# Kernel tuning notes

Hardware: AMD Instinct MI355X
Metric: run time of the kernel (lower is better)

The kernel has to match this reference:

```python
import jax, jax.numpy as jnp
import numpy as np

DEPTH = 4  # signature truncation depth
B, L, D = 64, 2048, 8  # batch, path length, channels


def _exp_levels(z, depth):
    """Restricted tensor exponential of a single linear increment.

    z: (B, d). Returns tuple of flattened z^{(x)k} / k!, shapes (B, d**k).
    """
    b = z.shape[0]
    levels = [z]
    for k in range(2, depth + 1):
        prev = levels[-1]  # (B, d**(k-1))
        levels.append((prev[:, :, None] * z[:, None, :]).reshape(b, -1) / k)
    return tuple(levels)


def _signature(path, depth):
    """Truncated path signature of a piecewise-linear path.

    Signature = product (in the truncated tensor algebra) of exp(increment_i),
    combined left-to-right via Chen's identity.
    path: (B, L, d) -> (B, d + d^2 + ... + d^depth)
    """
    inc = path[:, 1:, :] - path[:, :-1, :]  # (B, L-1, d)
    b = path.shape[0]

    def chen_mul_exp(A, z):
        # (A tensor-product exp(z)) truncated at `depth`.
        # C_k = A_k + e_k + sum_{j=1}^{k-1} A_{k-j} (x) e_j,  e_j = z^{(x)j}/j!
        e = _exp_levels(z, depth)
        out = []
        for k in range(1, depth + 1):
            c = A[k - 1] + e[k - 1]
            for j in range(1, k):
                c = c + (A[k - j - 1][:, :, None] * e[j - 1][:, None, :]).reshape(b, -1)
            out.append(c)
        return tuple(out)

    init = _exp_levels(inc[:, 0], depth)          # signature of first segment
    rest = jnp.swapaxes(inc[:, 1:], 0, 1)          # (L-2, B, d), scan over time
    final, _ = jax.lax.scan(lambda c, z: (chen_mul_exp(c, z), None), init, rest)
    return jnp.concatenate(final, axis=-1)         # flatten: (B, d + ... + d^depth)


def setup_inputs() -> dict:
    key = jax.random.key(0)
    path = jax.random.normal(key, (B, L, D), dtype=jnp.float32)
    return {"path": path}


def reference(path):
    return _signature(path, DEPTH)
```

## Files before the change

kernel.cpp:

```cpp
#include <hip/hip_runtime.h>

#define D8      8
#define LPATH   2048
#define NBATCH  64
#define NSTEPS  2047
#define NCHUNK  32
#define CSTEPS  64
#define SIGLEN  4680
#define OFF2    8
#define OFF3    72
#define OFF4    584
#define P4      68
#define SIGP    (OFF4 + 64 * P4)
#define APITCH  40

typedef float  f32x4 __attribute__((ext_vector_type(4)));
typedef short  s16x8 __attribute__((ext_vector_type(8)));

__device__ __forceinline__ void load8(const float* __restrict__ p, float* v) {
    float4 a = ((const float4*)p)[0];
    float4 b = ((const float4*)p)[1];
    v[0]=a.x; v[1]=a.y; v[2]=a.z; v[3]=a.w;
    v[4]=b.x; v[5]=b.y; v[6]=b.z; v[7]=b.w;
}
__device__ __forceinline__ void store8(float* __restrict__ p, const float* v) {
    ((float4*)p)[0] = make_float4(v[0],v[1],v[2],v[3]);
    ((float4*)p)[1] = make_float4(v[4],v[5],v[6],v[7]);
}
__device__ __forceinline__ unsigned int f2bf(float f) {
    unsigned int u = __builtin_bit_cast(unsigned int, f);
    u += 0x7FFFu + ((u >> 16) & 1u);
    return u >> 16;
}


__global__ __launch_bounds__(512) void sig_group_kernel(const float* __restrict__ path,
                                                        float* __restrict__ gsigs) {
    __shared__ __align__(16) float          zl[8][CSTEPS * D8];
    __shared__ __align__(16) unsigned short Al[8][64 * APITCH];
    __shared__ __align__(16) unsigned short Bl[8][64 * APITCH];
    __shared__ __align__(16) float          SB[SIGP];

    const int w    = threadIdx.x >> 6;
    const int lane = threadIdx.x & 63;
    const int G    = blockIdx.x & 3;
    const int b    = blockIdx.x >> 2;
    const int c    = G * 8 + w;
    const int t0   = c * CSTEPS;
    const int t1   = (t0 + CSTEPS < NSTEPS) ? (t0 + CSTEPS) : NSTEPS;
    const int n    = t1 - t0;
    const int i    = lane >> 3;
    const int j    = lane & 7;
    const float* __restrict__ pb = path + (size_t)b * LPATH * D8;

    {
        float4 z0, z1;
        if (lane < n) {
            const float* s0 = pb + (size_t)(t0 + lane) * D8;
            float4 a0 = ((const float4*)s0)[0], a1v = ((const float4*)s0)[1];
            float4 b0 = ((const float4*)(s0 + D8))[0], b1v = ((const float4*)(s0 + D8))[1];
            z0 = make_float4(b0.x - a0.x, b0.y - a0.y, b0.z - a0.z, b0.w - a0.w);
            z1 = make_float4(b1v.x - a1v.x, b1v.y - a1v.y, b1v.z - a1v.z, b1v.w - a1v.w);
        } else {
            z0 = make_float4(0.f, 0.f, 0.f, 0.f);
            z1 = z0;
        }
        ((float4*)(&zl[w][lane * D8]))[0] = z0;
        ((float4*)(&zl[w][lane * D8]))[1] = z1;
    }
    __syncthreads();

    const float Tj = pb[(size_t)t1 * D8 + j] - pb[(size_t)t0 * D8 + j];

    float A2 = 0.f, a1i = 0.f, Wl = Tj;
    float A3[8];
#pragma unroll
    for (int k = 0; k < 8; ++k) A3[k] = 0.f;
    f32x4 acc[4][4];
#pragma unroll
    for (int rt = 0; rt < 4; ++rt)
#pragma unroll
        for (int ct = 0; ct < 4; ++ct)
            acc[rt][ct] = (f32x4){0.f, 0.f, 0.f, 0.f};

    float* __restrict__ zw = &zl[w][0];
    unsigned short* __restrict__ Aw = &Al[w][0];
    unsigned short* __restrict__ Bw = &Bl[w][0];

    for (int pass = 0; pass < 4; ++pass) {
        const float* __restrict__ zp = zw + pass * 16 * D8;
#pragma unroll
        for (int bt = 0; bt < 2; ++bt) {
            unsigned int c3pk[4], c4pk[4], h3pk[4], h4pk[4];
#pragma unroll
            for (int e = 0; e < 8; ++e) {
                const int so = (bt * 8 + e) * D8;
                float4 za = *(const float4*)(zp + so);
                float4 zb = *(const float4*)(zp + so + 4);
                const float Z[8] = {za.x, za.y, za.z, za.w, zb.x, zb.y, zb.z, zb.w};
                const float Zi = zp[so + i];
                const float Zj = zp[so + j];

                const float p   = Zi * Zj;
                const float uq  = a1i * Zj;
                const float c4v = fmaf(uq, 1.f/6.f, fmaf(p, 1.f/24.f, A2 * 0.5f));
                const float c3v = fmaf(uq, 0.5f,    fmaf(p, 1.f/6.f,  A2));
                Wl -= Zj;
                const float h3v = Zi * Wl;
#pragma unroll
                for (int k = 0; k < 8; ++k) A3[k] = fmaf(c3v, Z[k], A3[k]);
                A2 = A2 + fmaf(p, 0.5f, uq);
                a1i += Zi;

                const unsigned int bc3 = f2bf(c3v), bc4 = f2bf(c4v);
                const unsigned int bh3 = f2bf(h3v), bh4 = f2bf(p);
                if ((e & 1) == 0) {
                    c3pk[e >> 1] = bc3; c4pk[e >> 1] = bc4;
                    h3pk[e >> 1] = bh3; h4pk[e >> 1] = bh4;
                } else {
                    c3pk[e >> 1] |= bc3 << 16; c4pk[e >> 1] |= bc4 << 16;
                    h3pk[e >> 1] |= bh3 << 16; h4pk[e >> 1] |= bh4 << 16;
                }
            }
            *(uint4*)(Aw + lane * APITCH + bt * 8)      = make_uint4(c3pk[0], c3pk[1], c3pk[2], c3pk[3]);
            *(uint4*)(Aw + lane * APITCH + 16 + bt * 8) = make_uint4(c4pk[0], c4pk[1], c4pk[2], c4pk[3]);
            *(uint4*)(Bw + lane * APITCH + bt * 8)      = make_uint4(h3pk[0], h3pk[1], h3pk[2], h3pk[3]);
            *(uint4*)(Bw + lane * APITCH + 16 + bt * 8) = make_uint4(h4pk[0], h4pk[1], h4pk[2], h4pk[3]);
        }
        s16x8 af[4], bfr[4];
#pragma unroll
        for (int rt = 0; rt < 4; ++rt)
            af[rt] = *(const s16x8*)(Aw + (rt * 16 + (lane & 15)) * APITCH + (lane >> 4) * 8);
#pragma unroll
        for (int ct = 0; ct < 4; ++ct)
            bfr[ct] = *(const s16x8*)(Bw + (ct * 16 + (lane & 15)) * APITCH + (lane >> 4) * 8);
#pragma unroll
        for (int rt = 0; rt < 4; ++rt)
#pragma unroll
            for (int ct = 0; ct < 4; ++ct)
                acc[rt][ct] = __builtin_amdgcn_mfma_f32_16x16x32_bf16(af[rt], bfr[ct], acc[rt][ct], 0, 0, 0);
    }

    const int r0 = (lane >> 4) * 4;
    const int cl = lane & 15;

    float FA4[8], fa3, FA1[8], FA2, fa1i;

    __syncthreads();
    for (int s = 0; s < 8; ++s) {
        if (w == s) {
            if ((lane & 7) == 0) SB[lane >> 3] = a1i;
            SB[OFF2 + lane] = A2;
#pragma unroll
            for (int k = 0; k < 8; ++k) SB[OFF3 + lane * 8 + k] = A3[k];
#pragma unroll
            for (int rt = 0; rt < 4; ++rt)
#pragma unroll
                for (int ct = 0; ct < 4; ++ct)
#pragma unroll
                    for (int reg = 0; reg < 4; ++reg)
                        SB[OFF4 + (rt * 16 + r0 + reg) * P4 + ct * 16 + cl] = acc[rt][ct][reg];
        }
        __syncthreads();
        if (s == 0) {
            load8(SB, FA1);
            fa1i = SB[i];
            FA2  = SB[OFF2 + lane];
            fa3  = SB[OFF3 + lane * 8 + w];
            load8(SB + OFF4 + lane * P4 + w * 8, FA4);
        } else {
            float B1[8]; load8(SB, B1);
            const float b1i = SB[i];
            const float b1j = SB[j];
            const float b2t = SB[OFF2 + lane];
            const float b1k = SB[w];
            const float b3k = SB[OFF3 + lane * 8 + w];
            const float b2jk = SB[OFF2 + j * 8 + w];
            float b4r[8], b2r[8], b3r[8];
            load8(SB + OFF4 + lane * P4 + w * 8, b4r);
            load8(SB + OFF2 + w * 8,             b2r);
            load8(SB + OFF3 + (j * 8 + w) * 8,   b3r);
#pragma unroll
            for (int l = 0; l < 8; ++l) {
                float v = FA4[l] + b4r[l];
                v = fmaf(fa3,  B1[l], v);
                v = fmaf(FA2,  b2r[l], v);
                FA4[l] = fmaf(fa1i, b3r[l], v);
            }
            fa3 = fmaf(fa1i, b2jk, fmaf(FA2, b1k, fa3 + b3k));
            FA2 = FA2 + fmaf(fa1i, b1j, b2t);
#pragma unroll
            for (int m = 0; m < 8; ++m) FA1[m] += B1[m];
            fa1i += b1i;
        }
        __syncthreads();
    }

    float* __restrict__ o = gsigs + (size_t)blockIdx.x * SIGLEN;
    if (w == 0) {
        if (lane < 8) o[lane] = FA1[lane];
        o[OFF2 + lane] = FA2;
    }
    o[OFF3 + lane * 8 + w] = fa3;
    store8(o + OFF4 + lane * 64 + w * 8, FA4);
}

struct BSet {
    float B1[8], b4r[8], b2r[8], b3r[8];
    float b1i, b1j, b2t, b1k, b3k, b2jk;
};

__device__ __forceinline__ void loadB(BSet& S, const float* __restrict__ B,
                                      int lane, int i, int j, int k) {
    load8(B, S.B1);
    S.b1i = B[i];
    S.b1j = B[j];
    S.b2t = B[OFF2 + lane];
    S.b1k = B[k];
    S.b3k = B[OFF3 + lane * 8 + k];
    S.b2jk = B[OFF2 + j * 8 + k];
    load8(B + OFF4 + lane * 64 + k * 8, S.b4r);
    load8(B + OFF2 + k * 8,             S.b2r);
    load8(B + OFF3 + j * 64 + k * 8,    S.b3r);
}

__device__ __forceinline__ void applyB(const BSet& S, float (&A4)[8], float& a3s,
                                       float (&A1)[8], float& A2, float& a1i) {
#pragma unroll
    for (int l = 0; l < 8; ++l) {
        float v = A4[l] + S.b4r[l];
        v = fmaf(a3s, S.B1[l], v);
        v = fmaf(A2,  S.b2r[l], v);
        A4[l] = fmaf(a1i, S.b3r[l], v);
    }
    a3s = fmaf(a1i, S.b2jk, fmaf(A2, S.b1k, a3s + S.b3k));
    A2 = A2 + fmaf(a1i, S.b1j, S.b2t);
#pragma unroll
    for (int m = 0; m < 8; ++m) A1[m] += S.B1[m];
    a1i += S.b1i;
}

template<int NPER>
__global__ __launch_bounds__(512) void sig_combine_kernel(const float* __restrict__ in,
                                                          float* __restrict__ out) {
    const int grp  = blockIdx.x;
    const int tid  = threadIdx.x;
    const int w    = tid >> 6;
    const int lane = tid & 63;
    const int i    = lane >> 3;
    const int j    = lane & 7;
    const int k    = w;
    const float* __restrict__ base = in + (size_t)grp * NPER * SIGLEN;

    float A4[8], a3s, A1[8], A2, a1i;
    load8(base, A1);
    a1i = base[i];
    A2  = base[OFF2 + lane];
    a3s = base[OFF3 + lane * 8 + k];
    load8(base + OFF4 + lane * 64 + k * 8, A4);

    BSet Sa, Sb;
    int s = 1;
    loadB(Sa, base + (size_t)s * SIGLEN, lane, i, j, k);
    while (s + 1 < NPER) {
        loadB(Sb, base + (size_t)(s + 1) * SIGLEN, lane, i, j, k);
        applyB(Sa, A4, a3s, A1, A2, a1i);
        ++s;
        if (s + 1 < NPER)
            loadB(Sa, base + (size_t)(s + 1) * SIGLEN, lane, i, j, k);
        applyB(Sb, A4, a3s, A1, A2, a1i);
        ++s;
    }
    if (s < NPER)
        applyB(Sa, A4, a3s, A1, A2, a1i);

    float* __restrict__ o = out + (size_t)grp * SIGLEN;
    if (w == 0) {
        if (lane < 8) o[lane] = A1[lane];
        o[OFF2 + lane] = A2;
    }
    o[OFF3 + lane * 8 + k] = a3s;
    store8(o + OFF4 + lane * 64 + k * 8, A4);
}

extern "C" void kernel_launch(void* const* d_in, const int* in_sizes, int n_in,
                              void* d_out, int out_size, void* d_ws, size_t ws_size,
                              hipStream_t stream) {
    const float* path = (const float*)d_in[0];
    float* out   = (float*)d_out;
    float* gsigs = (float*)d_ws;

    sig_group_kernel<<<NBATCH * 4, 512, 0, stream>>>(path, gsigs);
    sig_combine_kernel<4><<<NBATCH, 512, 0, stream>>>(gsigs, out);
}
```

Before: 31.36 us.

## Shrink chunks to 32 steps, use 4-wave blocks and packed bf16 conversion

Halves the steps per wave chunk and uses 4 waves per block, giving 16 groups per batch (1024 blocks of 256 threads) instead of 4 groups of 512 threads. The in-block combine now has each wave handle two k-slices, and the SB buffer reuses the Al shared region to cut LDS use, with launch bounds allowing 3 blocks per CU. The manual bf16 rounding is replaced by the v_cvt_pk_bf16_f32 instruction. The aim is more parallelism and occupancy in the first kernel, at the cost of a larger second combine stage over 16 group signatures. The __syncthreads after the z load is removed, which is safe only because each wave reads its own zl slice.

```diff
diff --git a/kernel.cpp b/kernel.cpp
--- a/kernel.cpp
+++ b/kernel.cpp
@@ -4,8 +4,8 @@
 #define LPATH   2048
 #define NBATCH  64
 #define NSTEPS  2047
-#define NCHUNK  32
-#define CSTEPS  64
+#define CSTEPS  32
+#define NCHUNK  64
 #define SIGLEN  4680
 #define OFF2    8
 #define OFF3    72
@@ -27,25 +27,50 @@
     ((float4*)p)[0] = make_float4(v[0],v[1],v[2],v[3]);
     ((float4*)p)[1] = make_float4(v[4],v[5],v[6],v[7]);
 }
-__device__ __forceinline__ unsigned int f2bf(float f) {
-    unsigned int u = __builtin_bit_cast(unsigned int, f);
-    u += 0x7FFFu + ((u >> 16) & 1u);
-    return u >> 16;
-}
-
-
-__global__ __launch_bounds__(512) void sig_group_kernel(const float* __restrict__ path,
-                                                        float* __restrict__ gsigs) {
-    __shared__ __align__(16) float          zl[8][CSTEPS * D8];
-    __shared__ __align__(16) unsigned short Al[8][64 * APITCH];
-    __shared__ __align__(16) unsigned short Bl[8][64 * APITCH];
-    __shared__ __align__(16) float          SB[SIGP];
+__device__ __forceinline__ unsigned int cvtpk(float lo, float hi) {
+    unsigned int r;
+    asm("v_cvt_pk_bf16_f32 %0, %1, %2" : "=v"(r) : "v"(lo), "v"(hi));
+    return r;
+}
+
+__device__ __forceinline__ void one_step(const float* __restrict__ zp, int so, int i, int j,
+                                         float& A2, float& a1i, float& Wl, float (&A3)[8],
+                                         float& c3o, float& c4o, float& h3o, float& h4o) {
+    float4 za = *(const float4*)(zp + so);
+    float4 zb = *(const float4*)(zp + so + 4);
+    const float Zi = zp[so + i];
+    const float Zj = zp[so + j];
+    const float p  = Zi * Zj;
+    const float uq = a1i * Zj;
+    c4o = fmaf(uq, 1.f/6.f, fmaf(p, 1.f/24.f, A2 * 0.5f));
+    c3o = fmaf(uq, 0.5f,    fmaf(p, 1.f/6.f,  A2));
+    Wl -= Zj;
+    h3o = Zi * Wl;
+    h4o = p;
+    A3[0] = fmaf(c3o, za.x, A3[0]);
+    A3[1] = fmaf(c3o, za.y, A3[1]);
+    A3[2] = fmaf(c3o, za.z, A3[2]);
+    A3[3] = fmaf(c3o, za.w, A3[3]);
+    A3[4] = fmaf(c3o, zb.x, A3[4]);
+    A3[5] = fmaf(c3o, zb.y, A3[5]);
+    A3[6] = fmaf(c3o, zb.z, A3[6]);
+    A3[7] = fmaf(c3o, zb.w, A3[7]);
+    A2 = A2 + fmaf(p, 0.5f, uq);
+    a1i += Zi;
+}
+
+__global__ __launch_bounds__(256, 3) void sig_group_kernel(const float* __restrict__ path,
+                                                           float* __restrict__ gsigs) {
+    __shared__ __align__(16) float          zl[4][CSTEPS * D8];
+    __shared__ __align__(16) unsigned short Al[4][64 * APITCH];
+    __shared__ __align__(16) unsigned short Bl[4][64 * APITCH];
+    float* SB = (float*)&Al[0][0];
 
     const int w    = threadIdx.x >> 6;
     const int lane = threadIdx.x & 63;
-    const int G    = blockIdx.x & 3;
-    const int b    = blockIdx.x >> 2;
-    const int c    = G * 8 + w;
+    const int G    = blockIdx.x & 15;
+    const int b    = blockIdx.x >> 4;
+    const int c    = G * 4 + w;
     const int t0   = c * CSTEPS;
     const int t1   = (t0 + CSTEPS < NSTEPS) ? (t0 + CSTEPS) : NSTEPS;
     const int n    = t1 - t0;
@@ -53,22 +78,18 @@
     const int j    = lane & 7;
     const float* __restrict__ pb = path + (size_t)b * LPATH * D8;
 
-    {
-        float4 z0, z1;
+    if (lane < CSTEPS) {
+        float4 z0 = make_float4(0.f,0.f,0.f,0.f), z1 = z0;
         if (lane < n) {
             const float* s0 = pb + (size_t)(t0 + lane) * D8;
             float4 a0 = ((const float4*)s0)[0], a1v = ((const float4*)s0)[1];
             float4 b0 = ((const float4*)(s0 + D8))[0], b1v = ((const float4*)(s0 + D8))[1];
             z0 = make_float4(b0.x - a0.x, b0.y - a0.y, b0.z - a0.z, b0.w - a0.w);
             z1 = make_float4(b1v.x - a1v.x, b1v.y - a1v.y, b1v.z - a1v.z, b1v.w - a1v.w);
-        } else {
-            z0 = make_float4(0.f, 0.f, 0.f, 0.f);
-            z1 = z0;
         }
         ((float4*)(&zl[w][lane * D8]))[0] = z0;
         ((float4*)(&zl[w][lane * D8]))[1] = z1;
     }
-    __syncthreads();
 
     const float Tj = pb[(size_t)t1 * D8 + j] - pb[(size_t)t0 * D8 + j];
 
@@ -83,44 +104,23 @@
         for (int ct = 0; ct < 4; ++ct)
             acc[rt][ct] = (f32x4){0.f, 0.f, 0.f, 0.f};
 
-    float* __restrict__ zw = &zl[w][0];
     unsigned short* __restrict__ Aw = &Al[w][0];
     unsigned short* __restrict__ Bw = &Bl[w][0];
 
-    for (int pass = 0; pass < 4; ++pass) {
-        const float* __restrict__ zp = zw + pass * 16 * D8;
+    for (int pass = 0; pass < 2; ++pass) {
+        const float* __restrict__ zp = &zl[w][0] + pass * 16 * D8;
 #pragma unroll
         for (int bt = 0; bt < 2; ++bt) {
             unsigned int c3pk[4], c4pk[4], h3pk[4], h4pk[4];
 #pragma unroll
-            for (int e = 0; e < 8; ++e) {
-                const int so = (bt * 8 + e) * D8;
-                float4 za = *(const float4*)(zp + so);
-                float4 zb = *(const float4*)(zp + so + 4);
-                const float Z[8] = {za.x, za.y, za.z, za.w, zb.x, zb.y, zb.z, zb.w};
-                const float Zi = zp[so + i];
-                const float Zj = zp[so + j];
-
-                const float p   = Zi * Zj;
-                const float uq  = a1i * Zj;
-                const float c4v = fmaf(uq, 1.f/6.f, fmaf(p, 1.f/24.f, A2 * 0.5f));
-                const float c3v = fmaf(uq, 0.5f,    fmaf(p, 1.f/6.f,  A2));
-                Wl -= Zj;
-                const float h3v = Zi * Wl;
-#pragma unroll
-                for (int k = 0; k < 8; ++k) A3[k] = fmaf(c3v, Z[k], A3[k]);
-                A2 = A2 + fmaf(p, 0.5f, uq);
-                a1i += Zi;
-
-                const unsigned int bc3 = f2bf(c3v), bc4 = f2bf(c4v);
-                const unsigned int bh3 = f2bf(h3v), bh4 = f2bf(p);
-                if ((e & 1) == 0) {
-                    c3pk[e >> 1] = bc3; c4pk[e >> 1] = bc4;
-                    h3pk[e >> 1] = bh3; h4pk[e >> 1] = bh4;
-                } else {
-                    c3pk[e >> 1] |= bc3 << 16; c4pk[e >> 1] |= bc4 << 16;
-                    h3pk[e >> 1] |= bh3 << 16; h4pk[e >> 1] |= bh4 << 16;
-                }
+            for (int pr = 0; pr < 4; ++pr) {
+                float c3a, c4a, h3a, h4a, c3b, c4b, h3b, h4b;
+                one_step(zp, (bt*8 + 2*pr)     * D8, i, j, A2, a1i, Wl, A3, c3a, c4a, h3a, h4a);
+                one_step(zp, (bt*8 + 2*pr + 1) * D8, i, j, A2, a1i, Wl, A3, c3b, c4b, h3b, h4b);
+                c3pk[pr] = cvtpk(c3a, c3b);
+                c4pk[pr] = cvtpk(c4a, c4b);
+                h3pk[pr] = cvtpk(h3a, h3b);
+                h4pk[pr] = cvtpk(h4a, h4b);
             }
             *(uint4*)(Aw + lane * APITCH + bt * 8)      = make_uint4(c3pk[0], c3pk[1], c3pk[2], c3pk[3]);
             *(uint4*)(Aw + lane * APITCH + 16 + bt * 8) = make_uint4(c4pk[0], c4pk[1], c4pk[2], c4pk[3]);
@@ -143,16 +143,16 @@
 
     const int r0 = (lane >> 4) * 4;
     const int cl = lane & 15;
-
-    float FA4[8], fa3, FA1[8], FA2, fa1i;
+    const int k0 = 2 * w;
+
+    float FA4[2][8], fa3[2], FA1[8], FA2, fa1i;
 
     __syncthreads();
-    for (int s = 0; s < 8; ++s) {
+    for (int s = 0; s < 4; ++s) {
         if (w == s) {
             if ((lane & 7) == 0) SB[lane >> 3] = a1i;
             SB[OFF2 + lane] = A2;
-#pragma unroll
-            for (int k = 0; k < 8; ++k) SB[OFF3 + lane * 8 + k] = A3[k];
+            store8(SB + OFF3 + lane * 8, A3);
 #pragma unroll
             for (int rt = 0; rt < 4; ++rt)
 #pragma unroll
@@ -166,28 +166,34 @@
             load8(SB, FA1);
             fa1i = SB[i];
             FA2  = SB[OFF2 + lane];
-            fa3  = SB[OFF3 + lane * 8 + w];
-            load8(SB + OFF4 + lane * P4 + w * 8, FA4);
+            fa3[0] = SB[OFF3 + lane * 8 + k0];
+            fa3[1] = SB[OFF3 + lane * 8 + k0 + 1];
+            load8(SB + OFF4 + lane * P4 + k0 * 8,       FA4[0]);
+            load8(SB + OFF4 + lane * P4 + (k0 + 1) * 8, FA4[1]);
         } else {
             float B1[8]; load8(SB, B1);
             const float b1i = SB[i];
             const float b1j = SB[j];
             const float b2t = SB[OFF2 + lane];
-            const float b1k = SB[w];
-            const float b3k = SB[OFF3 + lane * 8 + w];
-            const float b2jk = SB[OFF2 + j * 8 + w];
-            float b4r[8], b2r[8], b3r[8];
-            load8(SB + OFF4 + lane * P4 + w * 8, b4r);
-            load8(SB + OFF2 + w * 8,             b2r);
-            load8(SB + OFF3 + (j * 8 + w) * 8,   b3r);
-#pragma unroll
-            for (int l = 0; l < 8; ++l) {
-                float v = FA4[l] + b4r[l];
-                v = fmaf(fa3,  B1[l], v);
-                v = fmaf(FA2,  b2r[l], v);
-                FA4[l] = fmaf(fa1i, b3r[l], v);
+#pragma unroll
+            for (int kk = 0; kk < 2; ++kk) {
+                const int k = k0 + kk;
+                const float b1k  = SB[k];
+                const float b3k  = SB[OFF3 + lane * 8 + k];
+                const float b2jk = SB[OFF2 + j * 8 + k];
+                float b4r[8], b2r[8], b3r[8];
+                load8(SB + OFF4 + lane * P4 + k * 8, b4r);
+                load8(SB + OFF2 + k * 8,             b2r);
+                load8(SB + OFF3 + (j * 8 + k) * 8,   b3r);
+#pragma unroll
+                for (int l = 0; l < 8; ++l) {
+                    float v = FA4[kk][l] + b4r[l];
+                    v = fmaf(fa3[kk], B1[l], v);
+                    v = fmaf(FA2,     b2r[l], v);
+                    FA4[kk][l] = fmaf(fa1i, b3r[l], v);
+                }
+                fa3[kk] = fmaf(fa1i, b2jk, fmaf(FA2, b1k, fa3[kk] + b3k));
             }
-            fa3 = fmaf(fa1i, b2jk, fmaf(FA2, b1k, fa3 + b3k));
             FA2 = FA2 + fmaf(fa1i, b1j, b2t);
 #pragma unroll
             for (int m = 0; m < 8; ++m) FA1[m] += B1[m];
@@ -201,8 +207,9 @@
         if (lane < 8) o[lane] = FA1[lane];
         o[OFF2 + lane] = FA2;
     }
-    o[OFF3 + lane * 8 + w] = fa3;
-    store8(o + OFF4 + lane * 64 + w * 8, FA4);
+    *(float2*)(o + OFF3 + lane * 8 + k0) = make_float2(fa3[0], fa3[1]);
+    store8(o + OFF4 + lane * 64 + k0 * 8,       FA4[0]);
+    store8(o + OFF4 + lane * 64 + (k0 + 1) * 8, FA4[1]);
 }
 
 struct BSet {
@@ -290,6 +297,6 @@
     float* out   = (float*)d_out;
     float* gsigs = (float*)d_ws;
 
-    sig_group_kernel<<<NBATCH * 4, 512, 0, stream>>>(path, gsigs);
-    sig_combine_kernel<4><<<NBATCH, 512, 0, stream>>>(gsigs, out);
-}
+    sig_group_kernel<<<NBATCH * 16, 256, 0, stream>>>(path, gsigs);
+    sig_combine_kernel<16><<<NBATCH, 512, 0, stream>>>(gsigs, out);
+}
```

New measurement: 69.58 us. +121.9%, slower.

## Move level-3 accumulation into MFMA and transpose increments in shared memory

Applied to the files above, without the earlier changes.

Level-3 terms were accumulated with per-lane scalar FMAs over all eight channels. They are now computed by an extra MFMA column tile whose B operand is the bf16 increment vectors, padded with zero rows. Increments are stored channel-major with padding so each lane reads its Zi and Zj values as vector loads instead of scattered scalar reads, and the first block barrier is removed since each wave reads only its own data. The trade-offs are lower precision for level 3 (bf16 inputs instead of fp32), a fifth accumulator tile that raises register pressure, and extra MFMA work.

```diff
diff --git a/kernel.cpp b/kernel.cpp
--- a/kernel.cpp
+++ b/kernel.cpp
@@ -4,15 +4,17 @@
 #define LPATH   2048
 #define NBATCH  64
 #define NSTEPS  2047
+#define CSTEPS  64
 #define NCHUNK  32
-#define CSTEPS  64
 #define SIGLEN  4680
 #define OFF2    8
 #define OFF3    72
 #define OFF4    584
 #define P4      68
 #define SIGP    (OFF4 + 64 * P4)
+#define ZPITCH  68
 #define APITCH  40
+#define BROWS   80
 
 typedef float  f32x4 __attribute__((ext_vector_type(4)));
 typedef short  s16x8 __attribute__((ext_vector_type(8)));
@@ -33,12 +35,25 @@
     return u >> 16;
 }
 
+__device__ __forceinline__ void one_step(float Zi, float Zj,
+                                         float& A2, float& a1i, float& Wl,
+                                         float& c3o, float& c4o, float& h3o, float& h4o) {
+    const float p  = Zi * Zj;
+    const float uq = a1i * Zj;
+    c4o = fmaf(uq, 1.f/6.f, fmaf(p, 1.f/24.f, A2 * 0.5f));
+    c3o = fmaf(uq, 0.5f,    fmaf(p, 1.f/6.f,  A2));
+    Wl -= Zj;
+    h3o = Zi * Wl;
+    h4o = p;
+    A2 = A2 + fmaf(p, 0.5f, uq);
+    a1i += Zi;
+}
 
 __global__ __launch_bounds__(512) void sig_group_kernel(const float* __restrict__ path,
                                                         float* __restrict__ gsigs) {
-    __shared__ __align__(16) float          zl[8][CSTEPS * D8];
+    __shared__ __align__(16) float          zt[8][8 * ZPITCH];
     __shared__ __align__(16) unsigned short Al[8][64 * APITCH];
-    __shared__ __align__(16) unsigned short Bl[8][64 * APITCH];
+    __shared__ __align__(16) unsigned short Bl[8][BROWS * APITCH];
     __shared__ __align__(16) float          SB[SIGP];
 
     const int w    = threadIdx.x >> 6;
@@ -53,91 +68,88 @@
     const int j    = lane & 7;
     const float* __restrict__ pb = path + (size_t)b * LPATH * D8;
 
+    float* __restrict__ zw = &zt[w][0];
+    unsigned short* __restrict__ Aw = &Al[w][0];
+    unsigned short* __restrict__ Bw = &Bl[w][0];
+
     {
-        float4 z0, z1;
+        float z8[8];
         if (lane < n) {
             const float* s0 = pb + (size_t)(t0 + lane) * D8;
-            float4 a0 = ((const float4*)s0)[0], a1v = ((const float4*)s0)[1];
-            float4 b0 = ((const float4*)(s0 + D8))[0], b1v = ((const float4*)(s0 + D8))[1];
-            z0 = make_float4(b0.x - a0.x, b0.y - a0.y, b0.z - a0.z, b0.w - a0.w);
-            z1 = make_float4(b1v.x - a1v.x, b1v.y - a1v.y, b1v.z - a1v.z, b1v.w - a1v.w);
+            float a0[8], a1v[8];
+            load8(s0, a0); load8(s0 + D8, a1v);
+#pragma unroll
+            for (int m = 0; m < 8; ++m) z8[m] = a1v[m] - a0[m];
         } else {
-            z0 = make_float4(0.f, 0.f, 0.f, 0.f);
-            z1 = z0;
+#pragma unroll
+            for (int m = 0; m < 8; ++m) z8[m] = 0.f;
         }
-        ((float4*)(&zl[w][lane * D8]))[0] = z0;
-        ((float4*)(&zl[w][lane * D8]))[1] = z1;
-    }
-    __syncthreads();
+#pragma unroll
+        for (int m = 0; m < 8; ++m) zw[m * ZPITCH + lane] = z8[m];
+
+        const uint4 zz = make_uint4(0u, 0u, 0u, 0u);
+        *(uint4*)(Bw + 64 * APITCH + lane * 8) = zz;
+        if (lane < 16) *(uint4*)(Bw + 64 * APITCH + 512 + lane * 8) = zz;
+    }
 
     const float Tj = pb[(size_t)t1 * D8 + j] - pb[(size_t)t0 * D8 + j];
 
     float A2 = 0.f, a1i = 0.f, Wl = Tj;
-    float A3[8];
-#pragma unroll
-    for (int k = 0; k < 8; ++k) A3[k] = 0.f;
-    f32x4 acc[4][4];
+    f32x4 acc[4][5];
 #pragma unroll
     for (int rt = 0; rt < 4; ++rt)
 #pragma unroll
-        for (int ct = 0; ct < 4; ++ct)
+        for (int ct = 0; ct < 5; ++ct)
             acc[rt][ct] = (f32x4){0.f, 0.f, 0.f, 0.f};
 
-    float* __restrict__ zw = &zl[w][0];
-    unsigned short* __restrict__ Aw = &Al[w][0];
-    unsigned short* __restrict__ Bw = &Bl[w][0];
-
     for (int pass = 0; pass < 4; ++pass) {
-        const float* __restrict__ zp = zw + pass * 16 * D8;
+        const int p16 = pass * 16;
 #pragma unroll
         for (int bt = 0; bt < 2; ++bt) {
+            const int sb8 = p16 + bt * 8;
+            f32x4 zia = *(const f32x4*)(zw + i * ZPITCH + sb8);
+            f32x4 zib = *(const f32x4*)(zw + i * ZPITCH + sb8 + 4);
+            f32x4 zja = *(const f32x4*)(zw + j * ZPITCH + sb8);
+            f32x4 zjb = *(const f32x4*)(zw + j * ZPITCH + sb8 + 4);
+
             unsigned int c3pk[4], c4pk[4], h3pk[4], h4pk[4];
 #pragma unroll
-            for (int e = 0; e < 8; ++e) {
-                const int so = (bt * 8 + e) * D8;
-                float4 za = *(const float4*)(zp + so);
-                float4 zb = *(const float4*)(zp + so + 4);
-                const float Z[8] = {za.x, za.y, za.z, za.w, zb.x, zb.y, zb.z, zb.w};
-                const float Zi = zp[so + i];
-                const float Zj = zp[so + j];
-
-                const float p   = Zi * Zj;
-                const float uq  = a1i * Zj;
-                const float c4v = fmaf(uq, 1.f/6.f, fmaf(p, 1.f/24.f, A2 * 0.5f));
-                const float c3v = fmaf(uq, 0.5f,    fmaf(p, 1.f/6.f,  A2));
-                Wl -= Zj;
-                const float h3v = Zi * Wl;
-#pragma unroll
-                for (int k = 0; k < 8; ++k) A3[k] = fmaf(c3v, Z[k], A3[k]);
-                A2 = A2 + fmaf(p, 0.5f, uq);
-                a1i += Zi;
-
-                const unsigned int bc3 = f2bf(c3v), bc4 = f2bf(c4v);
-                const unsigned int bh3 = f2bf(h3v), bh4 = f2bf(p);
-                if ((e & 1) == 0) {
-                    c3pk[e >> 1] = bc3; c4pk[e >> 1] = bc4;
-                    h3pk[e >> 1] = bh3; h4pk[e >> 1] = bh4;
-                } else {
-                    c3pk[e >> 1] |= bc3 << 16; c4pk[e >> 1] |= bc4 << 16;
-                    h3pk[e >> 1] |= bh3 << 16; h4pk[e >> 1] |= bh4 << 16;
-                }
+            for (int t = 0; t < 4; ++t) {
+                const float Zi0 = (2*t   < 4) ? zia[(2*t)   & 3] : zib[(2*t)   & 3];
+                const float Zi1 = (2*t+1 < 4) ? zia[(2*t+1) & 3] : zib[(2*t+1) & 3];
+                const float Zj0 = (2*t   < 4) ? zja[(2*t)   & 3] : zjb[(2*t)   & 3];
+                const float Zj1 = (2*t+1 < 4) ? zja[(2*t+1) & 3] : zjb[(2*t+1) & 3];
+                float c3a, c4a, h3a, h4a, c3b, c4b, h3b, h4b;
+                one_step(Zi0, Zj0, A2, a1i, Wl, c3a, c4a, h3a, h4a);
+                one_step(Zi1, Zj1, A2, a1i, Wl, c3b, c4b, h3b, h4b);
+                c3pk[t] = f2bf(c3a) | (f2bf(c3b) << 16);
+                c4pk[t] = f2bf(c4a) | (f2bf(c4b) << 16);
+                h3pk[t] = f2bf(h3a) | (f2bf(h3b) << 16);
+                h4pk[t] = f2bf(h4a) | (f2bf(h4b) << 16);
             }
             *(uint4*)(Aw + lane * APITCH + bt * 8)      = make_uint4(c3pk[0], c3pk[1], c3pk[2], c3pk[3]);
             *(uint4*)(Aw + lane * APITCH + 16 + bt * 8) = make_uint4(c4pk[0], c4pk[1], c4pk[2], c4pk[3]);
             *(uint4*)(Bw + lane * APITCH + bt * 8)      = make_uint4(h3pk[0], h3pk[1], h3pk[2], h3pk[3]);
             *(uint4*)(Bw + lane * APITCH + 16 + bt * 8) = make_uint4(h4pk[0], h4pk[1], h4pk[2], h4pk[3]);
+            if (j == 0) {
+                const unsigned int z0 = f2bf(zia[0]) | (f2bf(zia[1]) << 16);
+                const unsigned int z1 = f2bf(zia[2]) | (f2bf(zia[3]) << 16);
+                const unsigned int z2 = f2bf(zib[0]) | (f2bf(zib[1]) << 16);
+                const unsigned int z3 = f2bf(zib[2]) | (f2bf(zib[3]) << 16);
+                *(uint4*)(Bw + (64 + i) * APITCH + bt * 8) = make_uint4(z0, z1, z2, z3);
+            }
         }
-        s16x8 af[4], bfr[4];
+        s16x8 af[4], bfr[5];
 #pragma unroll
         for (int rt = 0; rt < 4; ++rt)
             af[rt] = *(const s16x8*)(Aw + (rt * 16 + (lane & 15)) * APITCH + (lane >> 4) * 8);
 #pragma unroll
-        for (int ct = 0; ct < 4; ++ct)
+        for (int ct = 0; ct < 5; ++ct)
             bfr[ct] = *(const s16x8*)(Bw + (ct * 16 + (lane & 15)) * APITCH + (lane >> 4) * 8);
 #pragma unroll
         for (int rt = 0; rt < 4; ++rt)
 #pragma unroll
-            for (int ct = 0; ct < 4; ++ct)
+            for (int ct = 0; ct < 5; ++ct)
                 acc[rt][ct] = __builtin_amdgcn_mfma_f32_16x16x32_bf16(af[rt], bfr[ct], acc[rt][ct], 0, 0, 0);
     }
 
@@ -151,8 +163,13 @@
         if (w == s) {
             if ((lane & 7) == 0) SB[lane >> 3] = a1i;
             SB[OFF2 + lane] = A2;
-#pragma unroll
-            for (int k = 0; k < 8; ++k) SB[OFF3 + lane * 8 + k] = A3[k];
+            if (cl < 8) {
+#pragma unroll
+                for (int rt = 0; rt < 4; ++rt)
+#pragma unroll
+                    for (int reg = 0; reg < 4; ++reg)
+                        SB[OFF3 + (rt * 16 + r0 + reg) * 8 + cl] = acc[rt][4][reg];
+            }
 #pragma unroll
             for (int rt = 0; rt < 4; ++rt)
 #pragma unroll
```

After: 31.31 us (median of 2 runs). Within noise of the previous version (-0.2%).
